# Performance work log

Hardware: AMD Instinct MI355X
Metric: run time of the kernel (lower is better)

Reference implementation:

```python
import jax, jax.numpy as jnp
import numpy as np

B, S, HID = 2, 2048, 2048
NH, NKV, DH = 16, 4, 128
EPS = 1e-6

def rotate_half(x):
    x1, x2 = x[..., : x.shape[-1] // 2], x[..., x.shape[-1] // 2 :]
    return jnp.concatenate((-x2, x1), axis=-1)

def rms_norm(x, w):
    var = jnp.mean(jnp.square(x), axis=-1, keepdims=True)
    return w * (x * jax.lax.rsqrt(var + EPS))

def setup_inputs() -> dict:
    key = jax.random.key(0)
    ks = jax.random.split(key, 8)
    hidden_states = jax.random.normal(ks[0], (B, S, HID), dtype=jnp.float32)
    # causal additive mask, broadcastable to [B, H, S, S]
    causal = jnp.tril(jnp.ones((S, S), dtype=bool))
    attention_mask = jnp.where(causal, 0.0, -1e9).astype(jnp.float32)[None, None]
    # RoPE tables: [1, S, 1, DH] to broadcast over (B, S, H, DH)
    inv_freq = 1.0 / (10000.0 ** (np.arange(0, DH, 2, dtype=np.float32) / DH))
    t = np.arange(S, dtype=np.float32)
    freqs = np.einsum('s,d->sd', t, inv_freq)
    emb = np.concatenate([freqs, freqs], axis=-1)  # [S, DH]
    cos = jnp.asarray(np.cos(emb))[None, :, None, :]
    sin = jnp.asarray(np.sin(emb))[None, :, None, :]
    std = 0.02
    Wq = jax.random.normal(ks[1], (HID, NH * DH), dtype=jnp.float32) * std
    Wk = jax.random.normal(ks[2], (HID, NKV * DH), dtype=jnp.float32) * std
    Wv = jax.random.normal(ks[3], (HID, NKV * DH), dtype=jnp.float32) * std
    Wo = jax.random.normal(ks[4], (NH * DH, HID), dtype=jnp.float32) * std
    q_norm_w = jnp.ones((DH,), dtype=jnp.float32)
    k_norm_w = jnp.ones((DH,), dtype=jnp.float32)
    return dict(hidden_states=hidden_states, attention_mask=attention_mask,
                cos=cos, sin=sin, Wq=Wq, Wk=Wk, Wv=Wv, Wo=Wo,
                q_norm_w=q_norm_w, k_norm_w=k_norm_w)

def reference(hidden_states, attention_mask, cos, sin, Wq, Wk, Wv, Wo, q_norm_w, k_norm_w):
    b, s, _ = hidden_states.shape
    q = (hidden_states @ Wq).reshape(b, s, NH, DH)
    k = (hidden_states @ Wk).reshape(b, s, NKV, DH)
    v = (hidden_states @ Wv).reshape(b, s, NKV, DH)
    # per-head RMSNorm on q/k
    q = rms_norm(q, q_norm_w)
    k = rms_norm(k, k_norm_w)
    # RoPE
    q = q * cos + rotate_half(q) * sin
    k = k * cos + rotate_half(k) * sin
    # GQA: repeat kv heads
    groups = NH // NKV
    k = jnp.repeat(k, groups, axis=2)
    v = jnp.repeat(v, groups, axis=2)
    scale = 1.0 / jnp.sqrt(jnp.asarray(DH, dtype=q.dtype))
    scores = jnp.einsum('bqhd,bkhd->bhqk', q, k) * scale  # [B,H,S,S]
    scores = scores + attention_mask
    probs = jax.nn.softmax(scores, axis=-1)
    out = jnp.einsum('bhqk,bkhd->bqhd', probs, v)
    out = out.reshape(b, s, NH * DH)
    return out @ Wo
```

## Files before the change

### kernel.cpp

```cpp
#include <hip/hip_runtime.h>
#include <hip/hip_bf16.h>
#include <stdint.h>


typedef __attribute__((ext_vector_type(8))) short short8;
typedef __attribute__((ext_vector_type(4))) float floatx4;
typedef __hip_bfloat16 bf16_t;

#define MFMA16x16(a, b, c) __builtin_amdgcn_mfma_f32_16x16x32_bf16(a, b, c, 0, 0, 0)

__device__ __forceinline__ void async_copy16(const void* g, void* l) {
  __builtin_amdgcn_global_load_lds(
      (const __attribute__((address_space(1))) void*)g,
      (__attribute__((address_space(3))) void*)l, 16, 0, 0);
}

__device__ __forceinline__ unsigned short bf16bits(float x) {
  bf16_t h = __float2bfloat16(x);
  return *reinterpret_cast<unsigned short*>(&h);
}

__device__ __forceinline__ float fast_exp2(float x) {
  return __builtin_amdgcn_exp2f(x);
}

__global__ __launch_bounds__(256) void convbf_kernel(const float* __restrict__ in,
                                                     bf16_t* __restrict__ out, int n4) {
  int i = blockIdx.x * 256 + threadIdx.x;
  if (i < n4) {
    const float4 v = reinterpret_cast<const float4*>(in)[i];
    ushort4 o;
    o.x = bf16bits(v.x); o.y = bf16bits(v.y); o.z = bf16bits(v.z); o.w = bf16bits(v.w);
    reinterpret_cast<ushort4*>(out)[i] = o;
  }
}

__global__ __launch_bounds__(256) void wtrans_kernel(const float* __restrict__ W,
                                                     bf16_t* __restrict__ Wt, int N, int roff) {
  __shared__ float t[32][33];
  int k0 = blockIdx.y * 32, n0 = blockIdx.x * 32;
#pragma unroll
  for (int j = 0; j < 4; ++j)
    t[threadIdx.y + j * 8][threadIdx.x] =
        W[(size_t)(k0 + threadIdx.y + j * 8) * N + n0 + threadIdx.x];
  __syncthreads();
#pragma unroll
  for (int j = 0; j < 4; ++j) {
    int n = n0 + threadIdx.y + j * 8, k = k0 + threadIdx.x;
    Wt[(size_t)(roff + n) * 2048 + k] = __float2bfloat16(t[threadIdx.x][threadIdx.y + j * 8]);
  }
}

template <int OBF>
__global__ __launch_bounds__(256, 3) void gemm_bt_kernel(const bf16_t* __restrict__ A,
                                                         const bf16_t* __restrict__ Bt,
                                                         void* __restrict__ Cv,
                                                         int K, int ldc) {
  __shared__ __align__(16) char smem[32768];
  const int tid = threadIdx.x;
  const int wave = tid >> 6, lane = tid & 63;
  const int wr = wave >> 1, wc = wave & 1;
  const int l16 = lane & 15, lhi = lane >> 4;

  const int nwg = gridDim.x * gridDim.y;
  const int orig = blockIdx.y * gridDim.x + blockIdx.x;
  const int swz = (orig & 7) * (nwg >> 3) + (orig >> 3);
  const int bn = (swz % gridDim.x) * 128;
  const int bm = (swz / gridDim.x) * 128;

  floatx4 acc[4][4] = {};

  for (int k0 = 0; k0 < K; k0 += 64) {
    __syncthreads();
#pragma unroll
    for (int i = 0; i < 4; ++i) {
      int chunk = i * 4 + wave;
      unsigned p = (unsigned)chunk * 1024u + (unsigned)lane * 16u;
      unsigned row = p >> 7;
      unsigned colg = (p & 127u) ^ ((row & 7u) << 4);
      const char* gA = (const char*)(A + (size_t)(bm + row) * K + k0) + colg;
      async_copy16(gA, smem + (size_t)chunk * 1024);
      const char* gB = (const char*)(Bt + (size_t)(bn + row) * K + k0) + colg;
      async_copy16(gB, smem + 16384 + (size_t)chunk * 1024);
    }
    __syncthreads();
#pragma unroll
    for (int kk = 0; kk < 2; ++kk) {
      short8 fa[4], fb[4];
#pragma unroll
      for (int mi = 0; mi < 4; ++mi) {
        unsigned row = wr * 64 + mi * 16 + l16;
        unsigned off = row * 128u + kk * 64u + lhi * 16u;
        off ^= (row & 7u) << 4;
        fa[mi] = *(const short8*)(smem + off);
      }
#pragma unroll
      for (int ni = 0; ni < 4; ++ni) {
        unsigned row = wc * 64 + ni * 16 + l16;
        unsigned off = row * 128u + kk * 64u + lhi * 16u;
        off ^= (row & 7u) << 4;
        fb[ni] = *(const short8*)(smem + 16384 + off);
      }
#pragma unroll
      for (int mi = 0; mi < 4; ++mi)
#pragma unroll
        for (int ni = 0; ni < 4; ++ni)
          acc[mi][ni] = MFMA16x16(fa[mi], fb[ni], acc[mi][ni]);
    }
  }
#pragma unroll
  for (int mi = 0; mi < 4; ++mi)
#pragma unroll
    for (int ni = 0; ni < 4; ++ni)
#pragma unroll
      for (int r = 0; r < 4; ++r) {
        int row = bm + wr * 64 + mi * 16 + lhi * 4 + r;
        int col = bn + wc * 64 + ni * 16 + l16;
        if (OBF)
          ((bf16_t*)Cv)[(size_t)row * ldc + col] = __float2bfloat16(acc[mi][ni][r]);
        else
          ((float*)Cv)[(size_t)row * ldc + col] = acc[mi][ni][r];
      }
}

__global__ __launch_bounds__(256) void qknorm_rope_kernel(
    const bf16_t* __restrict__ Cqkv, const float* __restrict__ cosT,
    const float* __restrict__ sinT, const float* __restrict__ qw,
    const float* __restrict__ kw, bf16_t* __restrict__ Qa, bf16_t* __restrict__ Ka) {
  int wave = threadIdx.x >> 6, lane = threadIdx.x & 63;
  int task = blockIdx.x * 4 + wave;
  int unit = task % 20;
  int row = task / 20;
  int b = row >> 11, s = row & 2047;
  const bf16_t* src;
  const float* w;
  bf16_t* dst;
  float sc;
  if (unit < 16) {
    src = Cqkv + (size_t)row * 3072 + unit * 128;
    w = qw;
    dst = Qa + ((size_t)(b * 16 + unit) * 2048 + s) * 128;
    sc = 0.127517432f;
  } else {
    int kh = unit - 16;
    src = Cqkv + (size_t)row * 3072 + 2048 + kh * 128;
    w = kw;
    dst = Ka + ((size_t)(b * 4 + kh) * 2048 + s) * 128;
    sc = 1.0f;
  }
  float x1 = __bfloat162float(src[lane]), x2 = __bfloat162float(src[lane + 64]);
  float ss = x1 * x1 + x2 * x2;
#pragma unroll
  for (int off = 1; off < 64; off <<= 1) ss += __shfl_xor(ss, off, 64);
  float inv = rsqrtf(ss * (1.f / 128.f) + 1e-6f);
  x1 = x1 * inv * w[lane];
  x2 = x2 * inv * w[lane + 64];
  float c1 = cosT[(size_t)s * 128 + lane], c2 = cosT[(size_t)s * 128 + lane + 64];
  float s1 = sinT[(size_t)s * 128 + lane], s2 = sinT[(size_t)s * 128 + lane + 64];
  dst[lane] = __float2bfloat16((x1 * c1 - x2 * s1) * sc);
  dst[lane + 64] = __float2bfloat16((x2 * c2 + x1 * s2) * sc);
}

__global__ __launch_bounds__(256) void vtrans_kernel(const bf16_t* __restrict__ Cqkv,
                                                     bf16_t* __restrict__ Vt) {
  __shared__ bf16_t t[32][33];
  int bk = blockIdx.z;
  int b = bk >> 2, kh = bk & 3;
  int s0 = blockIdx.x * 32, d0 = blockIdx.y * 32;
  const bf16_t* src = Cqkv + (size_t)(b * 2048) * 3072 + 2560 + kh * 128;
#pragma unroll
  for (int j = 0; j < 4; ++j)
    t[threadIdx.y + j * 8][threadIdx.x] =
        src[(size_t)(s0 + threadIdx.y + j * 8) * 3072 + d0 + threadIdx.x];
  __syncthreads();
  bf16_t* dst = Vt + (size_t)(b * 4 + kh) * 128 * 2048;
#pragma unroll
  for (int j = 0; j < 4; ++j) {
    int d = d0 + threadIdx.y + j * 8, s = s0 + threadIdx.x;
    dst[(size_t)d * 2048 + s] = t[threadIdx.x][threadIdx.y + j * 8];
  }
}

__device__ __forceinline__ unsigned swz_row(unsigned row) {
  return (((row & 7u) ^ ((row >> 3) << 1)) & 7u) << 4;
}

__device__ __constant__ unsigned char kQbMap[32] = {
    31, 30, 29, 28, 27, 26, 25, 24,  0, 1, 2, 3, 4, 5, 6, 7,
    23, 22, 21, 20, 19, 18, 17, 16,  8, 9, 10, 11, 12, 13, 14, 15};

__global__ __launch_bounds__(256, 2) void flash_kernel(const bf16_t* __restrict__ Qa,
                                                       const bf16_t* __restrict__ Ka,
                                                       const bf16_t* __restrict__ Vt,
                                                       bf16_t* __restrict__ attnO) {
  __shared__ __align__(16) char smem[32768];
  const int tid = threadIdx.x;
  const int wave = tid >> 6, lane = tid & 63;
  const int l16 = lane & 15, lhi = lane >> 4;
  const int bid = blockIdx.x;
  const int bh = bid & 31;
  const int qb = kQbMap[bid >> 5];
  const int h = bh & 15, b = bh >> 4;
  const int kh = h >> 2;
  const int q0b = qb << 6;
  const int q0w = q0b + wave * 16;

  const bf16_t* Qb = Qa + ((size_t)bh * 2048 + q0w) * 128;
  const bf16_t* Kb = Ka + (size_t)(b * 4 + kh) * 2048 * 128;
  const bf16_t* Vb = Vt + (size_t)(b * 4 + kh) * 128 * 2048;

  char* Kl = smem;
  char* Vl = smem + 16384;

  short8 qf[4];
#pragma unroll
  for (int kk = 0; kk < 4; ++kk)
    qf[kk] = *(const short8*)(Qb + (size_t)l16 * 128 + kk * 32 + lhi * 8);

  short8 onesf;
#pragma unroll
  for (int j = 0; j < 8; ++j) onesf[j] = (short)0x3F80;

  floatx4 o[8] = {};
  floatx4 lsum = {};
  short8 pf[2];
  float m = -1e30f;

  const float THR = 11.5f;
  const int nch = qb + 1;

  auto stageK = [&](int key0) {
#pragma unroll
    for (int it = 0; it < 4; ++it) {
      unsigned p = (unsigned)(it * 4 + wave) * 1024u + (unsigned)lane * 16u;
      unsigned row = p >> 8;
      unsigned gcol = (p & 255u) ^ swz_row(row);
      async_copy16((const char*)(Kb + (size_t)(key0 + row) * 128) + gcol,
                   Kl + (size_t)(it * 4 + wave) * 1024);
    }
  };
  auto stageV = [&](int key0) {
#pragma unroll
    for (int it = 0; it < 4; ++it) {
      unsigned p = (unsigned)(it * 4 + wave) * 1024u + (unsigned)lane * 16u;
      unsigned row = p >> 7;
      unsigned gcol = (p & 127u) ^ swz_row(row);
      async_copy16((const char*)(Vb + (size_t)row * 2048 + key0) + gcol,
                   Vl + (size_t)(it * 4 + wave) * 1024);
    }
  };

  stageK(0);
  stageV(0);
  __syncthreads();

  for (int c = 0; c < nch; ++c) {
    const int kc0 = c << 6;

    floatx4 s[4] = {};
    __builtin_amdgcn_s_setprio(1);
#pragma unroll
    for (int g = 0; g < 4; ++g) {
      unsigned row = (unsigned)(l16 >> 2) * 8u + (unsigned)((g & 1) * 4) +
                     (unsigned)(l16 & 3) + (unsigned)((g >> 1) * 32);
      unsigned base = row * 256u;
      unsigned px = swz_row(row);
#pragma unroll
      for (int kk = 0; kk < 4; ++kk) {
        short8 kf = *(const short8*)(Kl + base + (((unsigned)(kk * 64 + lhi * 16)) ^ px));
        s[g] = MFMA16x16(kf, qf[kk], s[g]);
      }
    }
    __builtin_amdgcn_s_setprio(0);

    const int qrow = q0w + l16;
    if (kc0 + 64 > q0w) {
#pragma unroll
      for (int g = 0; g < 4; ++g)
#pragma unroll
        for (int r = 0; r < 4; ++r) {
          int key = kc0 + lhi * 8 + (g & 1) * 4 + r + (g >> 1) * 32;
          if (key > qrow) s[g][r] = -1e9f;
        }
    }
    float m0 = fmaxf(fmaxf(s[0][0], s[0][1]), fmaxf(s[0][2], s[0][3]));
    float m1 = fmaxf(fmaxf(s[1][0], s[1][1]), fmaxf(s[1][2], s[1][3]));
    float m2 = fmaxf(fmaxf(s[2][0], s[2][1]), fmaxf(s[2][2], s[2][3]));
    float m3 = fmaxf(fmaxf(s[3][0], s[3][1]), fmaxf(s[3][2], s[3][3]));
    float mx = fmaxf(fmaxf(m0, m1), fmaxf(m2, m3));
    mx = fmaxf(mx, __shfl_xor(mx, 16, 64));
    mx = fmaxf(mx, __shfl_xor(mx, 32, 64));
    bool grow = mx > m + THR;
    if (__any(grow)) {
      float mn = fmaxf(m, mx);
      float corr = fast_exp2(m - mn);
      m = mn;
#pragma unroll
      for (int r = 0; r < 4; ++r) {
        float co = __shfl(corr, lhi * 4 + r, 64);
        lsum[r] *= co;
#pragma unroll
        for (int f = 0; f < 8; ++f) o[f][r] *= co;
      }
    }
#pragma unroll
    for (int ks = 0; ks < 2; ++ks) {
      union { unsigned u[4]; short8 v; } pk;
#pragma unroll
      for (int half = 0; half < 2; ++half) {
        int g = ks * 2 + half;
        float p0 = fast_exp2(s[g][0] - m);
        float p1 = fast_exp2(s[g][1] - m);
        float p2 = fast_exp2(s[g][2] - m);
        float p3 = fast_exp2(s[g][3] - m);
        pk.u[half * 2] = (unsigned)bf16bits(p0) | ((unsigned)bf16bits(p1) << 16);
        pk.u[half * 2 + 1] = (unsigned)bf16bits(p2) | ((unsigned)bf16bits(p3) << 16);
      }
      pf[ks] = pk.v;
    }

    __syncthreads();

    if (c + 1 < nch) stageK((c + 1) << 6);

    __builtin_amdgcn_s_setprio(1);
#pragma unroll
    for (int ks = 0; ks < 2; ++ks) {
#pragma unroll
      for (int f = 0; f < 8; ++f) {
        unsigned row = (unsigned)(f * 16 + l16);
        short8 vf = *(const short8*)(Vl + row * 128u +
                                     (((unsigned)(ks * 64 + lhi * 16)) ^ swz_row(row)));
        o[f] = MFMA16x16(pf[ks], vf, o[f]);
      }
      lsum = MFMA16x16(pf[ks], onesf, lsum);
    }
    __builtin_amdgcn_s_setprio(0);

    __syncthreads();

    if (c + 1 < nch) stageV((c + 1) << 6);
  }

#pragma unroll
  for (int r = 0; r < 4; ++r) {
    float inv = 1.f / lsum[r];
    int row = q0w + lhi * 4 + r;
    size_t base = ((size_t)(b * 2048) + row) * 2048 + h * 128;
#pragma unroll
    for (int f = 0; f < 8; ++f)
      attnO[base + f * 16 + l16] = __float2bfloat16(o[f][r] * inv);
  }
}

extern "C" void kernel_launch(void* const* d_in, const int* in_sizes, int n_in,
                              void* d_out, int out_size, void* d_ws, size_t ws_size,
                              hipStream_t stream) {
  const float* hs = (const float*)d_in[0];
  const float* cosT = (const float*)d_in[2];
  const float* sinT = (const float*)d_in[3];
  const float* Wq = (const float*)d_in[4];
  const float* Wk = (const float*)d_in[5];
  const float* Wv = (const float*)d_in[6];
  const float* Wo = (const float*)d_in[7];
  const float* qw = (const float*)d_in[8];
  const float* kw = (const float*)d_in[9];
  float* out = (float*)d_out;

  char* ws = (char*)d_ws;
  size_t off = 0;
  auto alloc = [&](size_t bytes) {
    char* p = ws + off;
    off += (bytes + 255) & ~(size_t)255;
    return p;
  };
  bf16_t* hsb  = (bf16_t*)alloc((size_t)4096 * 2048 * 2);
  bf16_t* wqkv = (bf16_t*)alloc((size_t)3072 * 2048 * 2);
  bf16_t* wot  = (bf16_t*)alloc((size_t)2048 * 2048 * 2);
  bf16_t* cqkv = (bf16_t*)alloc((size_t)4096 * 3072 * 2);
  bf16_t* qa   = (bf16_t*)alloc((size_t)2 * 16 * 2048 * 128 * 2);
  bf16_t* ka   = (bf16_t*)alloc((size_t)2 * 4 * 2048 * 128 * 2);
  bf16_t* vt   = (bf16_t*)alloc((size_t)2 * 4 * 2048 * 128 * 2);
  bf16_t* attn = (bf16_t*)cqkv;

  convbf_kernel<<<8192, 256, 0, stream>>>(hs, hsb, 2097152);
  dim3 tb(32, 8);
  wtrans_kernel<<<dim3(64, 64), tb, 0, stream>>>(Wq, wqkv, 2048, 0);
  wtrans_kernel<<<dim3(16, 64), tb, 0, stream>>>(Wk, wqkv, 512, 2048);
  wtrans_kernel<<<dim3(16, 64), tb, 0, stream>>>(Wv, wqkv, 512, 2560);
  wtrans_kernel<<<dim3(64, 64), tb, 0, stream>>>(Wo, wot, 2048, 0);
  gemm_bt_kernel<1><<<dim3(24, 32), 256, 0, stream>>>(hsb, wqkv, cqkv, 2048, 3072);
  qknorm_rope_kernel<<<20480, 256, 0, stream>>>(cqkv, cosT, sinT, qw, kw, qa, ka);
  vtrans_kernel<<<dim3(64, 4, 8), tb, 0, stream>>>(cqkv, vt);
  flash_kernel<<<1024, 256, 0, stream>>>(qa, ka, vt, attn);
  gemm_bt_kernel<0><<<dim3(16, 32), 256, 0, stream>>>(attn, wot, out, 2048, 2048);
}
```

Before: 188.4 us.

## Fuse QK RMSNorm and RoPE into the QKV GEMM epilogue

The QKV projection GEMM epilogue now computes the per-head RMS norm with shuffles plus a shared-memory partial-sum exchange. It then applies RoPE using a shared-memory staging of the normalized tile to fetch the rotated partner column, and writes Q and K directly in head-major layout. V tiles go to a compact buffer for the transpose. This removes the separate qknorm_rope kernel and the round trip of the full QKV intermediate through global memory. In exchange it adds epilogue work, register pressure, a larger shared buffer, and uncoalesced 2-byte scattered stores in the GEMM.

```diff
diff --git a/kernel.cpp b/kernel.cpp
--- a/kernel.cpp
+++ b/kernel.cpp
@@ -51,12 +51,14 @@
   }
 }
 
-template <int OBF>
-__global__ __launch_bounds__(256, 3) void gemm_bt_kernel(const bf16_t* __restrict__ A,
-                                                         const bf16_t* __restrict__ Bt,
-                                                         void* __restrict__ Cv,
-                                                         int K, int ldc) {
-  __shared__ __align__(16) char smem[32768];
+template <int MODE>
+__global__ __launch_bounds__(256, 3) void gemm_bt_kernel(
+    const bf16_t* __restrict__ A, const bf16_t* __restrict__ Bt,
+    void* __restrict__ Cv, int K, int ldc,
+    const float* __restrict__ cosT, const float* __restrict__ sinT,
+    const float* __restrict__ qw, const float* __restrict__ kw,
+    bf16_t* __restrict__ Qa, bf16_t* __restrict__ Ka, bf16_t* __restrict__ Cvv) {
+  __shared__ __align__(16) char smem[33792];
   const int tid = threadIdx.x;
   const int wave = tid >> 6, lane = tid & 63;
   const int wr = wave >> 1, wc = wave & 1;
@@ -108,70 +110,132 @@
           acc[mi][ni] = MFMA16x16(fa[mi], fb[ni], acc[mi][ni]);
     }
   }
+
+  if (MODE == 0) {
+#pragma unroll
+    for (int mi = 0; mi < 4; ++mi)
+#pragma unroll
+      for (int ni = 0; ni < 4; ++ni)
+#pragma unroll
+        for (int r = 0; r < 4; ++r) {
+          int row = bm + wr * 64 + mi * 16 + lhi * 4 + r;
+          int col = bn + wc * 64 + ni * 16 + l16;
+          ((float*)Cv)[(size_t)row * ldc + col] = acc[mi][ni][r];
+        }
+    return;
+  }
+
+  const int unit = bn >> 7;
+  if (unit >= 20) {
+#pragma unroll
+    for (int mi = 0; mi < 4; ++mi)
+#pragma unroll
+      for (int ni = 0; ni < 4; ++ni)
+#pragma unroll
+        for (int r = 0; r < 4; ++r) {
+          int row = bm + wr * 64 + mi * 16 + lhi * 4 + r;
+          int col = (unit - 20) * 128 + wc * 64 + ni * 16 + l16;
+          Cvv[(size_t)row * 512 + col] = __float2bfloat16(acc[mi][ni][r]);
+        }
+    return;
+  }
+
+  __syncthreads();
+  float* ssbuf = (float*)smem;
+  char* xb = smem + 1024;
+
+  float ssp[4][4];
 #pragma unroll
   for (int mi = 0; mi < 4; ++mi)
 #pragma unroll
+    for (int r = 0; r < 4; ++r) {
+      float v = 0.f;
+#pragma unroll
+      for (int ni = 0; ni < 4; ++ni) v += acc[mi][ni][r] * acc[mi][ni][r];
+      ssp[mi][r] = v;
+    }
+#pragma unroll
+  for (int off = 1; off < 16; off <<= 1)
+#pragma unroll
+    for (int mi = 0; mi < 4; ++mi)
+#pragma unroll
+      for (int r = 0; r < 4; ++r) ssp[mi][r] += __shfl_xor(ssp[mi][r], off, 64);
+  if (l16 == 0) {
+#pragma unroll
+    for (int mi = 0; mi < 4; ++mi)
+#pragma unroll
+      for (int r = 0; r < 4; ++r)
+        ssbuf[wc * 128 + wr * 64 + mi * 16 + lhi * 4 + r] = ssp[mi][r];
+  }
+  __syncthreads();
+
+  const float* w = (unit < 16) ? qw : kw;
+  float wv[4];
+#pragma unroll
+  for (int ni = 0; ni < 4; ++ni) wv[ni] = w[wc * 64 + ni * 16 + l16];
+  float invs[4][4];
+#pragma unroll
+  for (int mi = 0; mi < 4; ++mi)
+#pragma unroll
+    for (int r = 0; r < 4; ++r) {
+      int rl = wr * 64 + mi * 16 + lhi * 4 + r;
+      float tot = ssp[mi][r] + ssbuf[(wc ^ 1) * 128 + rl];
+      invs[mi][r] = rsqrtf(tot * (1.f / 128.f) + 1e-6f);
+    }
+#pragma unroll
+  for (int mi = 0; mi < 4; ++mi)
+#pragma unroll
     for (int ni = 0; ni < 4; ++ni)
 #pragma unroll
       for (int r = 0; r < 4; ++r) {
-        int row = bm + wr * 64 + mi * 16 + lhi * 4 + r;
-        int col = bn + wc * 64 + ni * 16 + l16;
-        if (OBF)
-          ((bf16_t*)Cv)[(size_t)row * ldc + col] = __float2bfloat16(acc[mi][ni][r]);
-        else
-          ((float*)Cv)[(size_t)row * ldc + col] = acc[mi][ni][r];
-      }
-}
-
-__global__ __launch_bounds__(256) void qknorm_rope_kernel(
-    const bf16_t* __restrict__ Cqkv, const float* __restrict__ cosT,
-    const float* __restrict__ sinT, const float* __restrict__ qw,
-    const float* __restrict__ kw, bf16_t* __restrict__ Qa, bf16_t* __restrict__ Ka) {
-  int wave = threadIdx.x >> 6, lane = threadIdx.x & 63;
-  int task = blockIdx.x * 4 + wave;
-  int unit = task % 20;
-  int row = task / 20;
-  int b = row >> 11, s = row & 2047;
-  const bf16_t* src;
-  const float* w;
-  bf16_t* dst;
-  float sc;
-  if (unit < 16) {
-    src = Cqkv + (size_t)row * 3072 + unit * 128;
-    w = qw;
-    dst = Qa + ((size_t)(b * 16 + unit) * 2048 + s) * 128;
-    sc = 0.127517432f;
-  } else {
-    int kh = unit - 16;
-    src = Cqkv + (size_t)row * 3072 + 2048 + kh * 128;
-    w = kw;
-    dst = Ka + ((size_t)(b * 4 + kh) * 2048 + s) * 128;
-    sc = 1.0f;
-  }
-  float x1 = __bfloat162float(src[lane]), x2 = __bfloat162float(src[lane + 64]);
-  float ss = x1 * x1 + x2 * x2;
-#pragma unroll
-  for (int off = 1; off < 64; off <<= 1) ss += __shfl_xor(ss, off, 64);
-  float inv = rsqrtf(ss * (1.f / 128.f) + 1e-6f);
-  x1 = x1 * inv * w[lane];
-  x2 = x2 * inv * w[lane + 64];
-  float c1 = cosT[(size_t)s * 128 + lane], c2 = cosT[(size_t)s * 128 + lane + 64];
-  float s1 = sinT[(size_t)s * 128 + lane], s2 = sinT[(size_t)s * 128 + lane + 64];
-  dst[lane] = __float2bfloat16((x1 * c1 - x2 * s1) * sc);
-  dst[lane + 64] = __float2bfloat16((x2 * c2 + x1 * s2) * sc);
-}
-
-__global__ __launch_bounds__(256) void vtrans_kernel(const bf16_t* __restrict__ Cqkv,
+        int rl = wr * 64 + mi * 16 + lhi * 4 + r;
+        int col = wc * 64 + ni * 16 + l16;
+        float x = acc[mi][ni][r] * invs[mi][r] * wv[ni];
+        acc[mi][ni][r] = x;
+        unsigned byte = ((unsigned)rl * 256u + (unsigned)col * 2u) ^ ((unsigned)(rl & 7) << 4);
+        *(unsigned short*)(xb + byte) = bf16bits(x);
+      }
+  __syncthreads();
+
+  const float sc = (unit < 16) ? 0.127517432f : 1.0f;
+#pragma unroll
+  for (int mi = 0; mi < 4; ++mi)
+#pragma unroll
+    for (int r = 0; r < 4; ++r) {
+      int rl = wr * 64 + mi * 16 + lhi * 4 + r;
+      int rowg = bm + rl;
+      int b = rowg >> 11, s = rowg & 2047;
+      size_t dbase = (unit < 16)
+          ? ((size_t)(b * 16 + unit) * 2048 + s) * 128
+          : ((size_t)(b * 4 + unit - 16) * 2048 + s) * 128;
+      bf16_t* dp = (unit < 16) ? Qa : Ka;
+#pragma unroll
+      for (int ni = 0; ni < 4; ++ni) {
+        int col = wc * 64 + ni * 16 + l16;
+        int pcol = col ^ 64;
+        unsigned pb = ((unsigned)rl * 256u + (unsigned)pcol * 2u) ^ ((unsigned)(rl & 7) << 4);
+        unsigned short pu = *(unsigned short*)(xb + pb);
+        bf16_t pbf = *reinterpret_cast<bf16_t*>(&pu);
+        float xp = __bfloat162float(pbf);
+        float rot = (col < 64) ? -xp : xp;
+        float cs = cosT[(size_t)s * 128 + col];
+        float sn = sinT[(size_t)s * 128 + col];
+        dp[dbase + col] = __float2bfloat16((acc[mi][ni][r] * cs + rot * sn) * sc);
+      }
+    }
+}
+
+__global__ __launch_bounds__(256) void vtrans_kernel(const bf16_t* __restrict__ Cvv,
                                                      bf16_t* __restrict__ Vt) {
   __shared__ bf16_t t[32][33];
   int bk = blockIdx.z;
   int b = bk >> 2, kh = bk & 3;
   int s0 = blockIdx.x * 32, d0 = blockIdx.y * 32;
-  const bf16_t* src = Cqkv + (size_t)(b * 2048) * 3072 + 2560 + kh * 128;
+  const bf16_t* src = Cvv + (size_t)(b * 2048) * 512 + kh * 128;
 #pragma unroll
   for (int j = 0; j < 4; ++j)
     t[threadIdx.y + j * 8][threadIdx.x] =
-        src[(size_t)(s0 + threadIdx.y + j * 8) * 3072 + d0 + threadIdx.x];
+        src[(size_t)(s0 + threadIdx.y + j * 8) * 512 + d0 + threadIdx.x];
   __syncthreads();
   bf16_t* dst = Vt + (size_t)(b * 4 + kh) * 128 * 2048;
 #pragma unroll
@@ -377,11 +441,11 @@
   bf16_t* hsb  = (bf16_t*)alloc((size_t)4096 * 2048 * 2);
   bf16_t* wqkv = (bf16_t*)alloc((size_t)3072 * 2048 * 2);
   bf16_t* wot  = (bf16_t*)alloc((size_t)2048 * 2048 * 2);
-  bf16_t* cqkv = (bf16_t*)alloc((size_t)4096 * 3072 * 2);
+  bf16_t* cv   = (bf16_t*)alloc((size_t)4096 * 512 * 2);
   bf16_t* qa   = (bf16_t*)alloc((size_t)2 * 16 * 2048 * 128 * 2);
   bf16_t* ka   = (bf16_t*)alloc((size_t)2 * 4 * 2048 * 128 * 2);
   bf16_t* vt   = (bf16_t*)alloc((size_t)2 * 4 * 2048 * 128 * 2);
-  bf16_t* attn = (bf16_t*)cqkv;
+  bf16_t* attn = (bf16_t*)hsb;
 
   convbf_kernel<<<8192, 256, 0, stream>>>(hs, hsb, 2097152);
   dim3 tb(32, 8);
@@ -389,9 +453,11 @@
   wtrans_kernel<<<dim3(16, 64), tb, 0, stream>>>(Wk, wqkv, 512, 2048);
   wtrans_kernel<<<dim3(16, 64), tb, 0, stream>>>(Wv, wqkv, 512, 2560);
   wtrans_kernel<<<dim3(64, 64), tb, 0, stream>>>(Wo, wot, 2048, 0);
-  gemm_bt_kernel<1><<<dim3(24, 32), 256, 0, stream>>>(hsb, wqkv, cqkv, 2048, 3072);
-  qknorm_rope_kernel<<<20480, 256, 0, stream>>>(cqkv, cosT, sinT, qw, kw, qa, ka);
-  vtrans_kernel<<<dim3(64, 4, 8), tb, 0, stream>>>(cqkv, vt);
+  gemm_bt_kernel<2><<<dim3(24, 32), 256, 0, stream>>>(
+      hsb, wqkv, nullptr, 2048, 0, cosT, sinT, qw, kw, qa, ka, cv);
+  vtrans_kernel<<<dim3(64, 4, 8), tb, 0, stream>>>(cv, vt);
   flash_kernel<<<1024, 256, 0, stream>>>(qa, ka, vt, attn);
-  gemm_bt_kernel<0><<<dim3(16, 32), 256, 0, stream>>>(attn, wot, out, 2048, 2048);
-}
+  gemm_bt_kernel<0><<<dim3(16, 32), 256, 0, stream>>>(
+      attn, wot, out, 2048, 2048, nullptr, nullptr, nullptr, nullptr,
+      nullptr, nullptr, nullptr);
+}
```

Measured after the change: 191.9 us. About the same (+1.9%).
